# Kernel tuning notes

Measured on AMD Instinct MI355X. Metric: run time of the kernel, lower is better.

Reference implementation:

```python
import jax, jax.numpy as jnp
import numpy as np
import math

D = 1024  # output_dim (power of 2)
IN = 1024  # input dim
CAP = int(math.log2(D))  # number of butterfly stages


def _gen_indices(s):
    """Static FFT-butterfly index lists (numpy, computed at trace time)."""
    def ind_s(k):
        if k == 0:
            return [np.array([1, 0])]
        temp = np.arange(2 ** k)
        list0 = [np.concatenate([temp + 2 ** k, temp])]
        list1 = ind_s(k - 1)
        for i in range(k):
            list0.append(np.concatenate([list1[i], list1[i] + 2 ** k]))
        return list0

    t = ind_s(int(math.log2(s // 2)))
    cap = int(math.log2(s))
    ind_exe = [np.asarray(t[i], dtype=np.int32) for i in range(cap)]
    ind_param = []
    for i in range(cap):
        ind = np.concatenate([np.arange(0, s, 2 ** i) + j for j in range(2 ** i)]).astype(np.int32)
        ind_param.append(ind)
    return ind_exe, ind_param


IND_EXE, IND_PARAM = _gen_indices(D)


def setup_inputs() -> dict:
    key = jax.random.key(0)
    ks = jax.random.split(key, 9)
    B = 8192
    x = jax.random.normal(ks[0], (B, IN), dtype=jnp.float32)
    state = jax.random.normal(ks[1], (B, D), dtype=jnp.float32)
    theta = jax.random.uniform(ks[2], (CAP, D // 2), minval=-3.14, maxval=3.14, dtype=jnp.float32)
    U = jax.random.uniform(ks[3], (IN, 3 * D), minval=-0.01, maxval=0.01, dtype=jnp.float32)
    W_r = jax.random.uniform(ks[4], (D, D), minval=-0.01, maxval=0.01, dtype=jnp.float32)
    W_g = jax.random.uniform(ks[5], (D, D), minval=-0.01, maxval=0.01, dtype=jnp.float32)
    bias_r = jnp.full((D,), 2.0, dtype=jnp.float32)
    bias_g = jnp.zeros((D,), dtype=jnp.float32)
    bias_c = jnp.full((D,), 0.01, dtype=jnp.float32)
    return {"x": x, "state": state, "theta": theta, "U": U, "W_r": W_r,
            "W_g": W_g, "bias_r": bias_r, "bias_g": bias_g, "bias_c": bias_c}


def reference(x, state, theta, U, W_r, W_g, bias_r, bias_g, bias_c):
    # fft_param: rotation coefficients, permuted by the static ind_param lists
    cos_list = jnp.concatenate([jnp.cos(theta), jnp.cos(theta)], axis=1)   # [CAP, D]
    sin_list = jnp.concatenate([jnp.sin(theta), -jnp.sin(theta)], axis=1)  # [CAP, D]
    v1 = jnp.stack([cos_list[i][IND_PARAM[i]] for i in range(CAP)])  # [CAP, D]
    v2 = jnp.stack([sin_list[i][IND_PARAM[i]] for i in range(CAP)])  # [CAP, D]

    Ux = x @ U                                   # [B, 3D]
    U_cx, U_rx, U_gx = jnp.split(Ux, 3, axis=1)  # each [B, D]
    r = jax.nn.sigmoid(U_rx + state @ W_r + bias_r)
    g = jax.nn.sigmoid(U_gx + state @ W_g + bias_g)

    # butterfly orthogonal rotation of the state
    h = state
    for i in range(CAP):
        h = h * v1[i] + (h * v2[i])[:, IND_EXE[i]]

    # modReLU
    pre = r * h + U_cx
    c = jnp.sign(pre) * jax.nn.relu(jnp.abs(pre) + 0.001 + bias_c)

    out = g * state + (1.0 - g) * c
    return out
```

## Files before the change

kernel.cpp:

```cpp
#include <hip/hip_runtime.h>
#include <hip/hip_bf16.h>
#include <stdint.h>


typedef __bf16 bf16x8 __attribute__((ext_vector_type(8)));
typedef __bf16 bf16x4 __attribute__((ext_vector_type(4)));
typedef __bf16 bf16x2 __attribute__((ext_vector_type(2)));
typedef float f32x4 __attribute__((ext_vector_type(4)));

#define B_ROWS 8192

__device__ __forceinline__ void async16(__bf16* lds, const __hip_bfloat16* g) {
    __builtin_amdgcn_global_load_lds((const __attribute__((address_space(1))) void*)g,
                                     (__attribute__((address_space(3))) void*)lds,
                                     16, 0, 0);
}

__global__ __launch_bounds__(256) void prep_all(const float* __restrict__ x,
                                                const float* __restrict__ state,
                                                const float* __restrict__ theta,
                                                const float* __restrict__ U,
                                                const float* __restrict__ Wr,
                                                const float* __restrict__ Wg,
                                                __hip_bfloat16* __restrict__ xs,
                                                __hip_bfloat16* __restrict__ Wt0,
                                                __hip_bfloat16* __restrict__ Wt12,
                                                float* __restrict__ v1,
                                                float* __restrict__ v2) {
    __shared__ float tile[32][33];
    const int id = blockIdx.x;
    if (id < 8192) {
        const int row = id;
        const int col = threadIdx.x * 8;
        const float* src = (col < 1024) ? (x + (size_t)row * 1024 + col)
                                        : (state + (size_t)row * 1024 + (col - 1024));
        float4 a = *(const float4*)src;
        float4 b = *(const float4*)(src + 4);
        bf16x8 v;
        v[0] = (__bf16)a.x; v[1] = (__bf16)a.y; v[2] = (__bf16)a.z; v[3] = (__bf16)a.w;
        v[4] = (__bf16)b.x; v[5] = (__bf16)b.y; v[6] = (__bf16)b.z; v[7] = (__bf16)b.w;
        *(bf16x8*)((__bf16*)xs + (size_t)row * 2048 + col) = v;
    } else if (id < 13312) {
        const int wid = id - 8192;
        const float* src; int srcN, scol, sk;
        __hip_bfloat16* dst; int dstStride, dn, dk;
        bool ilv;
        if (wid < 1024) {
            int nx = wid & 31, ky = wid >> 5;
            src = U; srcN = 3072; scol = nx * 32; sk = ky * 32;
            dst = Wt0; dstStride = 1024; dn = nx * 32; dk = ky * 32;
            ilv = false;
        } else {
            int id2 = wid - 1024;
            int nx = id2 & 63, ky = id2 >> 6;
            int n0 = nx * 32, k0 = ky * 32;
            dst = Wt12; dstStride = 2048; dn = n0; dk = k0;
            ilv = true;
            if (k0 < 1024)      { src = U;  srcN = 3072; scol = 1024 + n0; sk = k0; }
            else if (n0 < 1024) { src = Wr; srcN = 1024; scol = n0;        sk = k0 - 1024; }
            else                { src = Wg; srcN = 1024; scol = n0 - 1024; sk = k0 - 1024; }
        }
        const int tx = threadIdx.x & 31, ty = threadIdx.x >> 5;
#pragma unroll
        for (int s = 0; s < 4; ++s)
            tile[ty + s * 8][tx] = src[(size_t)(sk + ty + s * 8) * srcN + scol + tx];
        __syncthreads();
#pragma unroll
        for (int s = 0; s < 4; ++s) {
            int n = dn + ty + s * 8;
            int wrow = ilv ? ((n < 1024) ? 2 * n : 2 * (n - 1024) + 1) : n;
            dst[(size_t)wrow * dstStride + dk + tx] = __float2bfloat16(tile[tx][ty + s * 8]);
        }
    } else {
        int idx = (id - 13312) * 256 + threadIdx.x;
        int i = idx >> 10;
        int j = idx & 1023;
        int Q = 1024 >> i;
        int j0 = j / Q;
        int m = j & (Q - 1);
        int q = (m << i) + j0;
        float th = theta[i * 512 + (q & 511)];
        float c = cosf(th);
        float s = sinf(th);
        v1[idx] = c;
        v2[idx] = (q < 512) ? s : -s;
    }
}

#define BAR()    asm volatile("s_barrier" ::: "memory")
#define LGKM(n)  asm volatile("s_waitcnt lgkmcnt(" #n ")" ::: "memory")
#define VMCNT(n) asm volatile("s_waitcnt vmcnt(" #n ")" ::: "memory")
#define SCHEDB() __builtin_amdgcn_sched_barrier(0)
#define PRIO1()  __builtin_amdgcn_s_setprio(1)
#define PRIO0()  __builtin_amdgcn_s_setprio(0)

__global__ __launch_bounds__(512, 2) void gemm_fused(const __hip_bfloat16* __restrict__ xs,
                                                     const __hip_bfloat16* __restrict__ Wt0,
                                                     const __hip_bfloat16* __restrict__ Wt12,
                                                     const float* __restrict__ bias_r,
                                                     const float* __restrict__ bias_g,
                                                     __hip_bfloat16* __restrict__ P) {
    __shared__ __align__(16) __bf16 As[2][16384];
    __shared__ __align__(16) __bf16 Bs[2][16384];

    const int bid = blockIdx.x;
    const int swz = (bid & 7) * 32 + (bid >> 3);
    const int nt = swz & 7;
    const int mt = swz >> 3;
    const int mBase = mt * 256;

    const int t = threadIdx.x;
    const int lane = t & 63;
    const int wv = t >> 6;
    const int wm = wv & 1;
    const int wn = wv >> 1;
    const int r0 = lane & 15;
    const int gq = lane >> 4;

    const int coff0 = ((gq ^ (r0 & 7)) << 3);
    const int coff1 = coff0 ^ 32;
    const int rowA = wm * 128 + r0;
    const int rowB = wn * 64 + r0;
    const int rowBu = wn * 32 + r0;

    const int s_row = t >> 3;
    const int s_q8 = (((t & 7) ^ (s_row & 7)) << 3);

    const __hip_bfloat16* Ag = xs + (size_t)(mBase + s_row) * 2048 + s_q8;
    const __hip_bfloat16* Bg = Wt12 + (size_t)(nt * 256 + s_row) * 2048 + s_q8;
    const __hip_bfloat16* Cg = Wt0 + (size_t)(nt * 128 + s_row) * 1024 + s_q8;

#define STG_A(buf, h, kt) do { \
    async16(&As[buf][(((h) << 10) + t) << 3],       Ag + (size_t)((h) * 128) * 2048 + (kt) * 64); \
    async16(&As[buf][(((h) << 10) + 512 + t) << 3], Ag + (size_t)((h) * 128 + 64) * 2048 + (kt) * 64); \
} while (0)
#define STG_B(buf, h, kt) do { \
    async16(&Bs[buf][(((h) << 10) + t) << 3],       Bg + (size_t)((h) * 128) * 2048 + (kt) * 64); \
    async16(&Bs[buf][(((h) << 10) + 512 + t) << 3], Bg + (size_t)((h) * 128 + 64) * 2048 + (kt) * 64); \
} while (0)
#define STG_C(buf, kt) do { \
    async16(&Bs[buf][t << 3],         Cg + (kt) * 64); \
    async16(&Bs[buf][(512 + t) << 3], Cg + (size_t)64 * 1024 + (kt) * 64); \
} while (0)

#define LOAD_AF(dst, bufArr, rbase) do { _Pragma("unroll") for (int i_ = 0; i_ < 4; ++i_) { \
    dst[i_][0] = *(const bf16x8*)&bufArr[((rbase) + i_ * 16) * 64 + coff0]; \
    dst[i_][1] = *(const bf16x8*)&bufArr[((rbase) + i_ * 16) * 64 + coff1]; } } while (0)
#define LOAD_BF(dst, bufArr, rbase) do { _Pragma("unroll") for (int j_ = 0; j_ < 2; ++j_) { \
    dst[j_][0] = *(const bf16x8*)&bufArr[((rbase) + j_ * 16) * 64 + coff0]; \
    dst[j_][1] = *(const bf16x8*)&bufArr[((rbase) + j_ * 16) * 64 + coff1]; } } while (0)
#define MFMA8(I0, J0, af, bf_) do { _Pragma("unroll") for (int i_ = 0; i_ < 4; ++i_) \
    _Pragma("unroll") for (int j_ = 0; j_ < 2; ++j_) { \
    acc[(I0) + i_][(J0) + j_] = __builtin_amdgcn_mfma_f32_16x16x32_bf16(af[i_][0], bf_[j_][0], acc[(I0) + i_][(J0) + j_], 0, 0, 0); \
    acc[(I0) + i_][(J0) + j_] = __builtin_amdgcn_mfma_f32_16x16x32_bf16(af[i_][1], bf_[j_][1], acc[(I0) + i_][(J0) + j_], 0, 0, 0); } } while (0)

    f32x4 acc[8][4];
    bf16x8 afl[4][2], afh[4][2], bb0[2][2], bb1[2][2];
    const f32x4 zero = {0.f, 0.f, 0.f, 0.f};
#pragma unroll
    for (int i = 0; i < 8; ++i)
#pragma unroll
        for (int j = 0; j < 4; ++j) acc[i][j] = zero;

    STG_A(0, 0, 0); STG_A(0, 1, 0);
    STG_B(0, 0, 0); STG_B(0, 1, 0);
    STG_A(1, 0, 1); STG_A(1, 1, 1);
    VMCNT(4);
    BAR();
    LOAD_AF(afl, As[0], rowA);
    LOAD_BF(bb0, Bs[0], rowB);

#pragma unroll 1
    for (int u = 0; u < 16; ++u) {
        const int kt1 = 2 * u + 1;
        const int kt2 = (2 * u + 2) & 31;
        const int kt3 = (2 * u + 3) & 31;

        LOAD_AF(afh, As[0], rowA + 64);
        STG_B(1, 0, kt1);
        BAR(); LGKM(8); SCHEDB();
        PRIO1(); MFMA8(0, 0, afl, bb0); PRIO0();
        BAR();
        LOAD_BF(bb1, Bs[0], rowB + 32);
        STG_B(1, 1, kt1);
        BAR(); LGKM(4); SCHEDB();
        PRIO1(); MFMA8(4, 0, afh, bb0); PRIO0();
        BAR();
        STG_A(0, 0, kt2);
        BAR(); LGKM(0); SCHEDB();
        PRIO1(); MFMA8(0, 2, afl, bb1); PRIO0();
        VMCNT(2);
        BAR();
        LOAD_AF(afl, As[1], rowA);
        LOAD_BF(bb0, Bs[1], rowB);
        STG_A(0, 1, kt2);
        BAR(); LGKM(12); SCHEDB();
        PRIO1(); MFMA8(4, 2, afh, bb1); PRIO0();
        BAR();
        LOAD_AF(afh, As[1], rowA + 64);
        STG_B(0, 0, kt2);
        BAR(); LGKM(8); SCHEDB();
        PRIO1(); MFMA8(0, 0, afl, bb0); PRIO0();
        BAR();
        LOAD_BF(bb1, Bs[1], rowB + 32);
        STG_B(0, 1, kt2);
        BAR(); LGKM(4); SCHEDB();
        PRIO1(); MFMA8(4, 0, afh, bb0); PRIO0();
        BAR();
        STG_A(1, 0, kt3);
        BAR(); LGKM(0); SCHEDB();
        PRIO1(); MFMA8(0, 2, afl, bb1); PRIO0();
        VMCNT(2);
        BAR();
        LOAD_AF(afl, As[0], rowA);
        LOAD_BF(bb0, Bs[0], rowB);
        STG_A(1, 1, kt3);
        BAR(); LGKM(12); SCHEDB();
        PRIO1(); MFMA8(4, 2, afh, bb1); PRIO0();
        BAR();
    }

    VMCNT(0);
    BAR();

    STG_A(0, 0, 0); STG_A(0, 1, 0);
    STG_C(0, 0);
    STG_C(1, 1);

    {
        float biasv[4];
#pragma unroll
        for (int j = 0; j < 4; ++j) {
            const int ct = nt * 256 + wn * 64 + j * 16 + r0;
            biasv[j] = (r0 & 1) ? bias_g[ct >> 1] : bias_r[ct >> 1];
        }
#pragma unroll
        for (int i = 0; i < 8; ++i) {
#pragma unroll
            for (int reg = 0; reg < 4; ++reg) {
                const int row = mBase + wm * 128 + i * 16 + gq * 4 + reg;
                __bf16* Pr = (__bf16*)P + (size_t)row * 3072 + 1024 + nt * 256 + wn * 64 + r0;
#pragma unroll
                for (int j = 0; j < 4; ++j) {
                    const float z = 1.0f / (1.0f + __expf(-(acc[i][j][reg] + biasv[j])));
                    Pr[j * 16] = (__bf16)z;
                }
            }
        }
    }

    VMCNT(0);
    BAR();

#pragma unroll
    for (int i = 0; i < 8; ++i)
#pragma unroll
        for (int j = 0; j < 2; ++j) acc[i][j] = zero;

#pragma unroll 1
    for (int u = 0; u < 8; ++u) {
        const int kt1 = 2 * u + 1;
        const int kt2 = (2 * u + 2) & 15;
        const int kt3 = (2 * u + 3) & 15;

        LOAD_AF(afl, As[0], rowA);
        LOAD_BF(bb0, Bs[0], rowBu);
        LOAD_AF(afh, As[0], rowA + 64);
        STG_A(1, 0, kt1); STG_A(1, 1, kt1);
        BAR(); LGKM(8); SCHEDB();
        PRIO1(); MFMA8(0, 0, afl, bb0); PRIO0();
        BAR();
        STG_C(0, kt2);
        BAR(); LGKM(0); SCHEDB();
        PRIO1(); MFMA8(4, 0, afh, bb0); PRIO0();
        VMCNT(2);
        BAR();
        LOAD_AF(afl, As[1], rowA);
        LOAD_BF(bb0, Bs[1], rowBu);
        LOAD_AF(afh, As[1], rowA + 64);
        STG_A(0, 0, kt2); STG_A(0, 1, kt2);
        BAR(); LGKM(8); SCHEDB();
        PRIO1(); MFMA8(0, 0, afl, bb0); PRIO0();
        BAR();
        STG_C(1, kt3);
        BAR(); LGKM(0); SCHEDB();
        PRIO1(); MFMA8(4, 0, afh, bb0); PRIO0();
        VMCNT(2);
        BAR();
    }

#pragma unroll
    for (int i = 0; i < 8; ++i) {
#pragma unroll
        for (int reg = 0; reg < 4; ++reg) {
            const int row = mBase + wm * 128 + i * 16 + gq * 4 + reg;
            __bf16* Pr = (__bf16*)P + (size_t)row * 3072 + nt * 128 + wn * 32 + r0;
#pragma unroll
            for (int j = 0; j < 2; ++j)
                Pr[j * 16] = (__bf16)(float)acc[i][j][reg];
        }
    }
    VMCNT(0);
}

#undef STG_A
#undef STG_B
#undef STG_C
#undef LOAD_AF
#undef LOAD_BF
#undef MFMA8

__global__ __launch_bounds__(256) void fuse_kernel(const float* __restrict__ state,
                                                   const __hip_bfloat16* __restrict__ P,
                                                   const float* __restrict__ v1,
                                                   const float* __restrict__ v2,
                                                   const float* __restrict__ bias_c,
                                                   float* __restrict__ out) {
    __shared__ float hbuf[8][1024];
    const int t = threadIdx.x;
    const int rowBase = blockIdx.x * 8;

    float h[8][4];
    float sv[8][4];
#pragma unroll
    for (int r = 0; r < 8; ++r) {
        float4 s4 = ((const float4*)(state + (size_t)(rowBase + r) * 1024))[t];
        h[r][0] = s4.x; h[r][1] = s4.y; h[r][2] = s4.z; h[r][3] = s4.w;
        sv[r][0] = s4.x; sv[r][1] = s4.y; sv[r][2] = s4.z; sv[r][3] = s4.w;
        *(float4*)&hbuf[r][4 * t] = s4;
    }

    {
        __syncthreads();
        float4 w1 = *(const float4*)&v1[4 * t];
        float4 w2 = *(const float4*)&v2[4 * (t ^ 128)];
        const float w1v[4] = {w1.x, w1.y, w1.z, w1.w};
        const float w2v[4] = {w2.x, w2.y, w2.z, w2.w};
#pragma unroll
        for (int r = 0; r < 8; ++r) {
            float4 pr = *(const float4*)&hbuf[r][4 * (t ^ 128)];
            const float pv[4] = {pr.x, pr.y, pr.z, pr.w};
#pragma unroll
            for (int e = 0; e < 4; ++e) h[r][e] = h[r][e] * w1v[e] + pv[e] * w2v[e];
        }
        __syncthreads();
    }
    {
#pragma unroll
        for (int r = 0; r < 8; ++r)
            *(float4*)&hbuf[r][4 * t] = (float4){h[r][0], h[r][1], h[r][2], h[r][3]};
        __syncthreads();
        float4 w1 = *(const float4*)&v1[1024 + 4 * t];
        float4 w2 = *(const float4*)&v2[1024 + 4 * (t ^ 64)];
        const float w1v[4] = {w1.x, w1.y, w1.z, w1.w};
        const float w2v[4] = {w2.x, w2.y, w2.z, w2.w};
#pragma unroll
        for (int r = 0; r < 8; ++r) {
            float4 pr = *(const float4*)&hbuf[r][4 * (t ^ 64)];
            const float pv[4] = {pr.x, pr.y, pr.z, pr.w};
#pragma unroll
            for (int e = 0; e < 4; ++e) h[r][e] = h[r][e] * w1v[e] + pv[e] * w2v[e];
        }
    }
#pragma unroll
    for (int i = 2; i <= 7; ++i) {
        const int H = 512 >> i;
        const int lm = H >> 2;
        float4 w1 = *(const float4*)&v1[i * 1024 + 4 * t];
        float4 w2 = *(const float4*)&v2[i * 1024 + 4 * (t ^ lm)];
        const float w1v[4] = {w1.x, w1.y, w1.z, w1.w};
        const float w2v[4] = {w2.x, w2.y, w2.z, w2.w};
#pragma unroll
        for (int r = 0; r < 8; ++r) {
#pragma unroll
            for (int e = 0; e < 4; ++e) {
                float p = __shfl_xor(h[r][e], lm, 64);
                h[r][e] = h[r][e] * w1v[e] + p * w2v[e];
            }
        }
    }
    {
        float4 w1 = *(const float4*)&v1[8 * 1024 + 4 * t];
        float4 w2 = *(const float4*)&v2[8 * 1024 + 4 * t];
        const float w1v[4] = {w1.x, w1.y, w1.z, w1.w};
        const float w2v[4] = {w2.x, w2.y, w2.z, w2.w};
#pragma unroll
        for (int r = 0; r < 8; ++r) {
            float nh[4];
#pragma unroll
            for (int e = 0; e < 4; ++e) nh[e] = h[r][e] * w1v[e] + h[r][e ^ 2] * w2v[e ^ 2];
#pragma unroll
            for (int e = 0; e < 4; ++e) h[r][e] = nh[e];
        }
        float4 u1 = *(const float4*)&v1[9 * 1024 + 4 * t];
        float4 u2 = *(const float4*)&v2[9 * 1024 + 4 * t];
        const float u1v[4] = {u1.x, u1.y, u1.z, u1.w};
        const float u2v[4] = {u2.x, u2.y, u2.z, u2.w};
#pragma unroll
        for (int r = 0; r < 8; ++r) {
            float nh[4];
#pragma unroll
            for (int e = 0; e < 4; ++e) nh[e] = h[r][e] * u1v[e] + h[r][e ^ 1] * u2v[e ^ 1];
#pragma unroll
            for (int e = 0; e < 4; ++e) h[r][e] = nh[e];
        }
    }

    const float4 bc = ((const float4*)bias_c)[t];
    const float bcv[4] = {bc.x, bc.y, bc.z, bc.w};
#pragma unroll
    for (int r = 0; r < 8; ++r) {
        const int row = rowBase + r;
        const __hip_bfloat16* Pr = P + (size_t)row * 3072;
        bf16x4 ux = *(const bf16x4*)((const __bf16*)Pr + 4 * t);
        bf16x8 rg = *(const bf16x8*)((const __bf16*)Pr + 1024 + 8 * t);
        float o[4];
#pragma unroll
        for (int e = 0; e < 4; ++e) {
            float Ucx = (float)ux[e];
            float rr  = (float)rg[2 * e];
            float gg  = (float)rg[2 * e + 1];
            float pre = rr * h[r][e] + Ucx;
            float mag = fabsf(pre) + 0.001f + bcv[e];
            float c = (pre > 0.f) ? mag : ((pre < 0.f) ? -mag : 0.f);
            o[e] = gg * sv[r][e] + (1.f - gg) * c;
        }
        ((float4*)(out + (size_t)row * 1024))[t] = (float4){o[0], o[1], o[2], o[3]};
    }
}

extern "C" void kernel_launch(void* const* d_in, const int* in_sizes, int n_in,
                              void* d_out, int out_size, void* d_ws, size_t ws_size,
                              hipStream_t stream) {
    const float* x      = (const float*)d_in[0];
    const float* state  = (const float*)d_in[1];
    const float* theta  = (const float*)d_in[2];
    const float* U      = (const float*)d_in[3];
    const float* W_r    = (const float*)d_in[4];
    const float* W_g    = (const float*)d_in[5];
    const float* bias_r = (const float*)d_in[6];
    const float* bias_g = (const float*)d_in[7];
    const float* bias_c = (const float*)d_in[8];
    float* out = (float*)d_out;

    __hip_bfloat16* xs   = (__hip_bfloat16*)d_ws;
    __hip_bfloat16* Wt0  = xs + (size_t)B_ROWS * 2048;
    __hip_bfloat16* Wt12 = Wt0 + (size_t)1024 * 1024;
    __hip_bfloat16* P    = Wt12 + (size_t)2048 * 2048;
    float* v1 = (float*)(P + (size_t)B_ROWS * 3072);
    float* v2 = v1 + 10 * 1024;

    prep_all<<<13352, 256, 0, stream>>>(x, state, theta, U, W_r, W_g, xs, Wt0, Wt12, v1, v2);
    gemm_fused<<<256, 512, 0, stream>>>(xs, Wt0, Wt12, bias_r, bias_g, P);
    fuse_kernel<<<1024, 256, 0, stream>>>(state, P, v1, v2, bias_c, out);
}
```

Before: 242.8 us.

## Restructure GEMM LDS pipeline with unified arena and triple-buffered second GEMM

Replaces the separate A/B LDS arrays with one shared arena and reorders the async global-to-LDS staging so each stage is split into finer halves issued earlier. This removes several barriers per iteration in the main gate GEMM. The second (U_c) GEMM becomes a rotating triple-buffered pipeline that prefetches two stages ahead. The prologue loads now overlap the sigmoid epilogue. LDS use rises to 144 KB per block, which may limit occupancy, and the reduced synchronisation risks read/write hazards if the wait counts are wrong.

```diff
diff --git a/kernel.cpp b/kernel.cpp
--- a/kernel.cpp
+++ b/kernel.cpp
@@ -100,8 +100,7 @@
                                                      const float* __restrict__ bias_r,
                                                      const float* __restrict__ bias_g,
                                                      __hip_bfloat16* __restrict__ P) {
-    __shared__ __align__(16) __bf16 As[2][16384];
-    __shared__ __align__(16) __bf16 Bs[2][16384];
+    __shared__ __align__(16) __bf16 arena[73728];
 
     const int bid = blockIdx.x;
     const int swz = (bid & 7) * 32 + (bid >> 3);
@@ -123,32 +122,43 @@
     const int rowB = wn * 64 + r0;
     const int rowBu = wn * 32 + r0;
 
-    const int s_row = t >> 3;
-    const int s_q8 = (((t & 7) ^ (s_row & 7)) << 3);
-
-    const __hip_bfloat16* Ag = xs + (size_t)(mBase + s_row) * 2048 + s_q8;
-    const __hip_bfloat16* Bg = Wt12 + (size_t)(nt * 256 + s_row) * 2048 + s_q8;
-    const __hip_bfloat16* Cg = Wt0 + (size_t)(nt * 128 + s_row) * 1024 + s_q8;
-
-#define STG_A(buf, h, kt) do { \
-    async16(&As[buf][(((h) << 10) + t) << 3],       Ag + (size_t)((h) * 128) * 2048 + (kt) * 64); \
-    async16(&As[buf][(((h) << 10) + 512 + t) << 3], Ag + (size_t)((h) * 128 + 64) * 2048 + (kt) * 64); \
-} while (0)
-#define STG_B(buf, h, kt) do { \
-    async16(&Bs[buf][(((h) << 10) + t) << 3],       Bg + (size_t)((h) * 128) * 2048 + (kt) * 64); \
-    async16(&Bs[buf][(((h) << 10) + 512 + t) << 3], Bg + (size_t)((h) * 128 + 64) * 2048 + (kt) * 64); \
-} while (0)
-#define STG_C(buf, kt) do { \
-    async16(&Bs[buf][t << 3],         Cg + (kt) * 64); \
-    async16(&Bs[buf][(512 + t) << 3], Cg + (size_t)64 * 1024 + (kt) * 64); \
-} while (0)
-
-#define LOAD_AF(dst, bufArr, rbase) do { _Pragma("unroll") for (int i_ = 0; i_ < 4; ++i_) { \
-    dst[i_][0] = *(const bf16x8*)&bufArr[((rbase) + i_ * 16) * 64 + coff0]; \
-    dst[i_][1] = *(const bf16x8*)&bufArr[((rbase) + i_ * 16) * 64 + coff1]; } } while (0)
-#define LOAD_BF(dst, bufArr, rbase) do { _Pragma("unroll") for (int j_ = 0; j_ < 2; ++j_) { \
-    dst[j_][0] = *(const bf16x8*)&bufArr[((rbase) + j_ * 16) * 64 + coff0]; \
-    dst[j_][1] = *(const bf16x8*)&bufArr[((rbase) + j_ * 16) * 64 + coff1]; } } while (0)
+    const int u = t >> 3;
+    const int sq = (((t & 7) ^ (u & 7)) << 3);
+    const int rB = (u & 31) + ((u >> 5) << 6);
+    const int ldsB = rB * 64 + ((t & 7) << 3);
+
+    const __hip_bfloat16* Ag = xs + (size_t)(mBase + u) * 2048 + sq;
+    const __hip_bfloat16* BgB = Wt12 + (size_t)(nt * 256 + rB) * 2048 + sq;
+    const __hip_bfloat16* CgB = Wt0 + (size_t)(nt * 128 + u) * 1024 + sq;
+
+#define A0OFF 0
+#define A1OFF 16384
+#define B0OFF 32768
+#define B1OFF 49152
+
+#define STG(ldsoff, gaddr) async16(&arena[ldsoff], gaddr)
+#define STG_AH0(AOFF, kt) do { \
+    STG((AOFF) + (t << 3),            Ag + (size_t)(kt) * 64); \
+    STG((AOFF) + 4096 + (t << 3),     Ag + (size_t)64 * 2048 + (size_t)(kt) * 64); } while (0)
+#define STG_AH1(AOFF, kt) do { \
+    STG((AOFF) + 8192 + (t << 3),     Ag + (size_t)128 * 2048 + (size_t)(kt) * 64); \
+    STG((AOFF) + 12288 + (t << 3),    Ag + (size_t)192 * 2048 + (size_t)(kt) * 64); } while (0)
+#define STG_B0(BOFF, kt) do { \
+    STG((BOFF) + ldsB,                BgB + (size_t)(kt) * 64); \
+    STG((BOFF) + ldsB + 8192,         BgB + (size_t)128 * 2048 + (size_t)(kt) * 64); } while (0)
+#define STG_B1(BOFF, kt) do { \
+    STG((BOFF) + ldsB + 2048,         BgB + (size_t)32 * 2048 + (size_t)(kt) * 64); \
+    STG((BOFF) + ldsB + 10240,        BgB + (size_t)160 * 2048 + (size_t)(kt) * 64); } while (0)
+#define STG_C2(COFF, kt) do { \
+    STG((COFF) + (t << 3),            CgB + (size_t)(kt) * 64); \
+    STG((COFF) + 4096 + (t << 3),     CgB + (size_t)64 * 1024 + (size_t)(kt) * 64); } while (0)
+
+#define LOAD_AF(dst, AOFF, rbase) do { _Pragma("unroll") for (int i_ = 0; i_ < 4; ++i_) { \
+    dst[i_][0] = *(const bf16x8*)&arena[(AOFF) + ((rbase) + i_ * 16) * 64 + coff0]; \
+    dst[i_][1] = *(const bf16x8*)&arena[(AOFF) + ((rbase) + i_ * 16) * 64 + coff1]; } } while (0)
+#define LOAD_BF(dst, BOFF, rbase) do { _Pragma("unroll") for (int j_ = 0; j_ < 2; ++j_) { \
+    dst[j_][0] = *(const bf16x8*)&arena[(BOFF) + ((rbase) + j_ * 16) * 64 + coff0]; \
+    dst[j_][1] = *(const bf16x8*)&arena[(BOFF) + ((rbase) + j_ * 16) * 64 + coff1]; } } while (0)
 #define MFMA8(I0, J0, af, bf_) do { _Pragma("unroll") for (int i_ = 0; i_ < 4; ++i_) \
     _Pragma("unroll") for (int j_ = 0; j_ < 2; ++j_) { \
     acc[(I0) + i_][(J0) + j_] = __builtin_amdgcn_mfma_f32_16x16x32_bf16(af[i_][0], bf_[j_][0], acc[(I0) + i_][(J0) + j_], 0, 0, 0); \
@@ -162,70 +172,68 @@
 #pragma unroll
         for (int j = 0; j < 4; ++j) acc[i][j] = zero;
 
-    STG_A(0, 0, 0); STG_A(0, 1, 0);
-    STG_B(0, 0, 0); STG_B(0, 1, 0);
-    STG_A(1, 0, 1); STG_A(1, 1, 1);
+    STG_AH0(A0OFF, 0); STG_AH1(A0OFF, 0);
+    STG_B0(B0OFF, 0);  STG_B1(B0OFF, 0);
+    STG_B0(B1OFF, 1);
+    STG_AH0(A1OFF, 1);
     VMCNT(4);
     BAR();
-    LOAD_AF(afl, As[0], rowA);
-    LOAD_BF(bb0, Bs[0], rowB);
+    LOAD_AF(afl, A0OFF, rowA);
+    LOAD_BF(bb0, B0OFF, rowB);
 
 #pragma unroll 1
-    for (int u = 0; u < 16; ++u) {
-        const int kt1 = 2 * u + 1;
-        const int kt2 = (2 * u + 2) & 31;
-        const int kt3 = (2 * u + 3) & 31;
-
-        LOAD_AF(afh, As[0], rowA + 64);
-        STG_B(1, 0, kt1);
+    for (int uu = 0; uu < 16; ++uu) {
+        const int k1 = 2 * uu + 1;
+        const int k2 = (2 * uu + 2) & 31;
+        const int k3 = (2 * uu + 3) & 31;
+
+        LOAD_AF(afh, A0OFF, rowA + 64);
+        STG_AH1(A1OFF, k1);
+        STG_B1(B1OFF, k1);
         BAR(); LGKM(8); SCHEDB();
         PRIO1(); MFMA8(0, 0, afl, bb0); PRIO0();
-        BAR();
-        LOAD_BF(bb1, Bs[0], rowB + 32);
-        STG_B(1, 1, kt1);
+        LOAD_BF(bb1, B0OFF, rowB + 32);
         BAR(); LGKM(4); SCHEDB();
         PRIO1(); MFMA8(4, 0, afh, bb0); PRIO0();
-        BAR();
-        STG_A(0, 0, kt2);
+        STG_B0(B0OFF, k2);
+        VMCNT(2);
         BAR(); LGKM(0); SCHEDB();
         PRIO1(); MFMA8(0, 2, afl, bb1); PRIO0();
-        VMCNT(2);
-        BAR();
-        LOAD_AF(afl, As[1], rowA);
-        LOAD_BF(bb0, Bs[1], rowB);
-        STG_A(0, 1, kt2);
-        BAR(); LGKM(12); SCHEDB();
+        LOAD_AF(afl, A1OFF, rowA);
+        LOAD_BF(bb0, B1OFF, rowB);
+        STG_AH0(A0OFF, k2);
+        BAR(); SCHEDB();
         PRIO1(); MFMA8(4, 2, afh, bb1); PRIO0();
-        BAR();
-        LOAD_AF(afh, As[1], rowA + 64);
-        STG_B(0, 0, kt2);
+        LOAD_AF(afh, A1OFF, rowA + 64);
+        STG_AH1(A0OFF, k2);
+        STG_B1(B0OFF, k2);
         BAR(); LGKM(8); SCHEDB();
         PRIO1(); MFMA8(0, 0, afl, bb0); PRIO0();
-        BAR();
-        LOAD_BF(bb1, Bs[1], rowB + 32);
-        STG_B(0, 1, kt2);
+        LOAD_BF(bb1, B1OFF, rowB + 32);
         BAR(); LGKM(4); SCHEDB();
         PRIO1(); MFMA8(4, 0, afh, bb0); PRIO0();
-        BAR();
-        STG_A(1, 0, kt3);
+        STG_B0(B1OFF, k3);
+        VMCNT(2);
         BAR(); LGKM(0); SCHEDB();
         PRIO1(); MFMA8(0, 2, afl, bb1); PRIO0();
-        VMCNT(2);
-        BAR();
-        LOAD_AF(afl, As[0], rowA);
-        LOAD_BF(bb0, Bs[0], rowB);
-        STG_A(1, 1, kt3);
-        BAR(); LGKM(12); SCHEDB();
+        LOAD_AF(afl, A0OFF, rowA);
+        LOAD_BF(bb0, B0OFF, rowB);
+        STG_AH0(A1OFF, k3);
+        BAR(); SCHEDB();
         PRIO1(); MFMA8(4, 2, afh, bb1); PRIO0();
-        BAR();
-    }
-
-    VMCNT(0);
+    }
+
+    LGKM(0); VMCNT(0);
     BAR();
 
-    STG_A(0, 0, 0); STG_A(0, 1, 0);
-    STG_C(0, 0);
-    STG_C(1, 1);
+#define UA0 0
+#define UA1 16384
+#define UA2 32768
+#define UC0 49152
+#define UC1 57344
+#define UC2 65536
+    STG_AH0(UA0, 0); STG_AH1(UA0, 0); STG_C2(UC0, 0);
+    STG_C2(UC1, 1); STG_AH0(UA1, 1); STG_AH1(UA1, 1);
 
     {
         float biasv[4];
@@ -249,44 +257,47 @@
         }
     }
 
-    VMCNT(0);
+    VMCNT(6);
     BAR();
+    LOAD_AF(afl, UA0, rowA);
+    LOAD_BF(bb0, UC0, rowBu);
 
 #pragma unroll
     for (int i = 0; i < 8; ++i)
 #pragma unroll
         for (int j = 0; j < 2; ++j) acc[i][j] = zero;
 
+    int aR0 = UA0, aR1 = UA1, aS = UA2;
+    int cR0 = UC0, cR1 = UC1, cS = UC2;
+
 #pragma unroll 1
-    for (int u = 0; u < 8; ++u) {
-        const int kt1 = 2 * u + 1;
-        const int kt2 = (2 * u + 2) & 15;
-        const int kt3 = (2 * u + 3) & 15;
-
-        LOAD_AF(afl, As[0], rowA);
-        LOAD_BF(bb0, Bs[0], rowBu);
-        LOAD_AF(afh, As[0], rowA + 64);
-        STG_A(1, 0, kt1); STG_A(1, 1, kt1);
+    for (int kt = 0; kt < 16; kt += 2) {
+        const int ka2 = (kt + 2) & 15;
+        const int ka3 = (kt + 3) & 15;
+
+        LOAD_AF(afh, aR0, rowA + 64);
+        STG_C2(cS, ka2);
+        VMCNT(2);
         BAR(); LGKM(8); SCHEDB();
         PRIO1(); MFMA8(0, 0, afl, bb0); PRIO0();
-        BAR();
-        STG_C(0, kt2);
-        BAR(); LGKM(0); SCHEDB();
+        LOAD_AF(afl, aR1, rowA);
+        LOAD_BF(bb1, cR1, rowBu);
+        STG_AH0(aS, ka2); STG_AH1(aS, ka2);
+        BAR(); LGKM(12); SCHEDB();
         PRIO1(); MFMA8(4, 0, afh, bb0); PRIO0();
+        LOAD_AF(afh, aR1, rowA + 64);
+        STG_C2(cR0, ka3);
         VMCNT(2);
-        BAR();
-        LOAD_AF(afl, As[1], rowA);
-        LOAD_BF(bb0, Bs[1], rowBu);
-        LOAD_AF(afh, As[1], rowA + 64);
-        STG_A(0, 0, kt2); STG_A(0, 1, kt2);
         BAR(); LGKM(8); SCHEDB();
-        PRIO1(); MFMA8(0, 0, afl, bb0); PRIO0();
-        BAR();
-        STG_C(1, kt3);
-        BAR(); LGKM(0); SCHEDB();
-        PRIO1(); MFMA8(4, 0, afh, bb0); PRIO0();
-        VMCNT(2);
-        BAR();
+        PRIO1(); MFMA8(0, 0, afl, bb1); PRIO0();
+        LOAD_AF(afl, aS, rowA);
+        LOAD_BF(bb0, cS, rowBu);
+        STG_AH0(aR0, ka3); STG_AH1(aR0, ka3);
+        BAR(); LGKM(12); SCHEDB();
+        PRIO1(); MFMA8(4, 0, afh, bb1); PRIO0();
+
+        int ta = aR1; aR1 = aR0; aR0 = aS; aS = ta;
+        int tc = cR1; cR1 = cR0; cR0 = cS; cS = tc;
     }
 
 #pragma unroll
@@ -303,9 +314,12 @@
     VMCNT(0);
 }
 
-#undef STG_A
-#undef STG_B
-#undef STG_C
+#undef STG
+#undef STG_AH0
+#undef STG_AH1
+#undef STG_B0
+#undef STG_B1
+#undef STG_C2
 #undef LOAD_AF
 #undef LOAD_BF
 #undef MFMA8
```

Measured after the change: 271.4 us. 1.12x slower.
